# Optimization experiments

Hardware: AMD Instinct MI355X
Metric: run time of the kernel (lower is better)

## Reference

```python
import jax, jax.numpy as jnp
import numpy as np

EPS = 1e-07
B, N = 128, 512


def setup_inputs() -> dict:
    key = jax.random.key(0)
    k1, k2, k3 = jax.random.split(key, 3)
    pred = jax.random.normal(k1, (B, N), dtype=jnp.float32)
    target = jax.random.uniform(k2, (B, N), dtype=jnp.float32)  # survival times in (0,1)
    valid_mask = jax.random.bernoulli(k3, p=0.9, shape=(B, N))  # bool
    return {"pred": pred, "target": target, "valid_mask": valid_mask}


def reference(pred, target, valid_mask):
    # pred, target: (B, N) float32; valid_mask: (B, N) bool
    n = pred.shape[1]
    target_masked = jnp.where(valid_mask, target, jnp.float32(-1.0))  # (B, N)
    T_i = target_masked[:, :, None]  # (B, N, 1)
    T_j = target_masked[:, None, :]  # (B, 1, N)
    batch_max_time = jnp.max(target_masked, axis=1, keepdims=True)[:, :, None]  # (B, 1, 1)

    # player i is eliminated (not the final survivor) and valid
    is_elimination = (T_i < batch_max_time) & (T_i > 0) & valid_mask[:, :, None]  # (B, N, 1)
    # risk set at time t_i: players j still alive (T_j >= T_i) and valid
    risk_set_mask = (T_j >= T_i) & valid_mask[:, None, :]  # (B, N, N)

    pred_j = pred[:, None, :]  # (B, 1, N)
    risk_pred_masked = jnp.where(risk_set_mask, pred_j, -jnp.inf)  # (B, N, N)
    log_denominator = jax.nn.logsumexp(risk_pred_masked, axis=2, keepdims=True)  # (B, N, 1)
    log_probs = pred_j - log_denominator  # (B, N, N)

    # part 1: -log p of the eliminated player itself (diagonal)
    log_prob_eliminated = jnp.diagonal(log_probs, axis1=1, axis2=2)[:, :, None]  # (B, N, 1)
    loss_part1 = -log_prob_eliminated * is_elimination

    # part 2: -log(1 - p_i) for survivors i in risk set (excluding eliminated)
    probs = jnp.exp(log_probs)
    eye = jnp.eye(n, dtype=bool)[None]  # (1, N, N)
    surviving_mask = risk_set_mask & ~eye
    probs_clamped = jnp.minimum(probs, 1.0 - EPS)
    loss_surviving = -jnp.log(1.0 - probs_clamped + EPS)
    loss_part2 = jnp.sum(loss_surviving * surviving_mask.astype(pred.dtype), axis=2, keepdims=True)
    loss_part2 = loss_part2 * is_elimination

    total_loss_per_batch = jnp.sum(loss_part1 + loss_part2, axis=1)  # (B, 1)
    valid_batch_mask = (jnp.sum(valid_mask, axis=1) >= 2).astype(pred.dtype)  # (B,)
    final_loss = jnp.sum(jnp.squeeze(total_loss_per_batch, axis=1) * valid_batch_mask)
    num_valid = jnp.maximum(jnp.sum(valid_batch_mask), 1.0)
    return final_loss / num_valid
```

## Files before the change

kernel.cpp:

```cpp
#include <hip/hip_runtime.h>
#include <math.h>

#define BB 128
#define NN 512
#define CHUNKS 8
#define RPB (NN / CHUNKS)
#define RPW (RPB / 4)
#define GRID (BB * CHUNKS)
#define EPSF 1e-7f
#define ONEP (1.0f + EPSF)
#define TWOEPS (2.0f * EPSF)

__global__ __launch_bounds__(256) void cox_main(const float* __restrict__ pred,
                                                const float* __restrict__ target,
                                                const int* __restrict__ valid,
                                                float* __restrict__ ws) {
    __shared__ float s_e[NN];
    __shared__ float s_tm[NN];
    __shared__ float s_p[NN];
    __shared__ float s_is[NN];
    __shared__ float s_max[4];
    __shared__ float s_cnt[4];
    __shared__ float s_acc[4];

    const int b     = blockIdx.x / CHUNKS;
    const int chunk = blockIdx.x % CHUNKS;
    const int tid   = threadIdx.x;
    const int lane  = tid & 63;
    const int wave  = tid >> 6;

    float lmax = -1.0f, lcnt = 0.0f;
    #pragma unroll
    for (int k = 0; k < NN / 256; ++k) {
        int j = tid + 256 * k;
        float p = pred[b * NN + j];
        float t = target[b * NN + j];
        int   v = valid[b * NN + j];
        float tm = v ? t : -1.0f;
        s_p[j]  = p;
        s_e[j]  = __expf(p);
        s_tm[j] = tm;
        lmax = fmaxf(lmax, tm);
        lcnt += v ? 1.0f : 0.0f;
    }
    #pragma unroll
    for (int off = 32; off; off >>= 1) {
        lmax = fmaxf(lmax, __shfl_xor(lmax, off, 64));
        lcnt += __shfl_xor(lcnt, off, 64);
    }
    if (lane == 0) { s_max[wave] = lmax; s_cnt[wave] = lcnt; }
    __syncthreads();
    const float bmax = fmaxf(fmaxf(s_max[0], s_max[1]), fmaxf(s_max[2], s_max[3]));
    const float bcnt = s_cnt[0] + s_cnt[1] + s_cnt[2] + s_cnt[3];
    const float batch_valid = (bcnt >= 2.0f) ? 1.0f : 0.0f;

    float tj[8], e0[8];
    #pragma unroll
    for (int k = 0; k < 8; ++k) {
        tj[k] = s_tm[lane + 64 * k];
        e0[k] = s_e[lane + 64 * k];
    }

    float acc = 0.0f;
    const int row0 = chunk * RPB + wave * RPW;
    for (int r = 0; r < RPW; ++r) {
        const int i = row0 + r;
        const float Ti = s_tm[i];
        if (!(Ti > 0.0f && Ti < bmax)) continue;

        float em[8];
        float S = 0.0f;
        #pragma unroll
        for (int k = 0; k < 8; ++k) {
            float x = (tj[k] >= Ti) ? e0[k] : 0.0f;
            em[k] = x;
            S += x;
        }
        #pragma unroll
        for (int off = 32; off; off >>= 1) S += __shfl_xor(S, off, 64);
        const float invS = __builtin_amdgcn_rcpf(S);
        if (lane == 0) s_is[i] = invS;

        float prod = 1.0f;
        #pragma unroll
        for (int k = 0; k < 8; ++k)
            prod *= fmaxf(fmaf(-em[k], invS, ONEP), TWOEPS);
        acc -= __logf(prod);
    }

    if (lane < RPW) {
        const int i = row0 + lane;
        const float Ti = s_tm[i];
        if (Ti > 0.0f && Ti < bmax) {
            float invS = s_is[i];
            float part1 = -__logf(invS) - s_p[i];
            float pii = s_e[i] * invS;
            float qi = fmaxf(ONEP - pii, TWOEPS);
            acc += part1 + __logf(qi);
        }
    }

    #pragma unroll
    for (int off = 32; off; off >>= 1) acc += __shfl_xor(acc, off, 64);
    if (lane == 0) s_acc[wave] = acc;
    __syncthreads();
    if (tid == 0) {
        ws[blockIdx.x] = (s_acc[0] + s_acc[1] + s_acc[2] + s_acc[3]) * batch_valid;
        if (chunk == 0) ws[GRID + b] = batch_valid;
    }
}

__global__ __launch_bounds__(256) void cox_final(const float* __restrict__ ws,
                                                 float* __restrict__ out) {
    __shared__ float s_tot[4];
    __shared__ float s_cnt[4];
    const int tid  = threadIdx.x;
    const int lane = tid & 63;
    const int wave = tid >> 6;

    float tot = 0.0f;
    #pragma unroll
    for (int k = 0; k < GRID / 256; ++k) tot += ws[tid + 256 * k];
    float cnt = (tid < BB) ? ws[GRID + tid] : 0.0f;

    #pragma unroll
    for (int off = 32; off; off >>= 1) {
        tot += __shfl_xor(tot, off, 64);
        cnt += __shfl_xor(cnt, off, 64);
    }
    if (lane == 0) { s_tot[wave] = tot; s_cnt[wave] = cnt; }
    __syncthreads();
    if (tid == 0) {
        float T = s_tot[0] + s_tot[1] + s_tot[2] + s_tot[3];
        float C = s_cnt[0] + s_cnt[1] + s_cnt[2] + s_cnt[3];
        out[0] = T / fmaxf(C, 1.0f);
    }
}

extern "C" void kernel_launch(void* const* d_in, const int* in_sizes, int n_in,
                              void* d_out, int out_size, void* d_ws, size_t ws_size,
                              hipStream_t stream) {
    const float* pred   = (const float*)d_in[0];
    const float* target = (const float*)d_in[1];
    const int*   valid  = (const int*)d_in[2];
    float* out = (float*)d_out;
    float* ws  = (float*)d_ws;

    cox_main<<<GRID, 256, 0, stream>>>(pred, target, valid, ws);
    cox_final<<<1, 256, 0, stream>>>(ws, out);
}
```

Baseline: 69.29 us.

## Fold diagonal term into per-row product and process two rows branch-free

Computes the diagonal -log p_i and the +log q_i correction inside the main row loop. It does this by multiplying a factor F = invS*e_i/q_ii into the lane that owns column i, so only one log per lane per row is needed. This removes the s_p/s_is shared arrays and the separate epilogue pass. Rows are processed two at a time without the early-continue, using masking (Ti=inf, elim weight) to give more ILP across the shuffle reductions. In exchange it computes full work for non-eliminated rows, adds an extra rcp per row, and combines the terms in a different floating-point order.

New measurement: 68.95 us. About the same (-0.5%).

```diff
diff --git a/kernel.cpp b/kernel.cpp
--- a/kernel.cpp
+++ b/kernel.cpp
@@ -17,8 +17,6 @@
                                                 float* __restrict__ ws) {
     __shared__ float s_e[NN];
     __shared__ float s_tm[NN];
-    __shared__ float s_p[NN];
-    __shared__ float s_is[NN];
     __shared__ float s_max[4];
     __shared__ float s_cnt[4];
     __shared__ float s_acc[4];
@@ -37,7 +35,6 @@
         float t = target[b * NN + j];
         int   v = valid[b * NN + j];
         float tm = v ? t : -1.0f;
-        s_p[j]  = p;
         s_e[j]  = __expf(p);
         s_tm[j] = tm;
         lmax = fmaxf(lmax, tm);
@@ -63,40 +60,56 @@
 
     float acc = 0.0f;
     const int row0 = chunk * RPB + wave * RPW;
-    for (int r = 0; r < RPW; ++r) {
-        const int i = row0 + r;
-        const float Ti = s_tm[i];
-        if (!(Ti > 0.0f && Ti < bmax)) continue;
-
-        float em[8];
-        float S = 0.0f;
+    for (int r0 = 0; r0 < RPW; r0 += 2) {
+        float Ti[2], ei[2], elim[2], S[2], prod[2];
+        float em[2][8];
+        #pragma unroll
+        for (int rr = 0; rr < 2; ++rr) {
+            const int i = row0 + r0 + rr;
+            float t = s_tm[i];
+            bool el = (t > 0.0f && t < bmax);
+            elim[rr] = el ? 1.0f : 0.0f;
+            Ti[rr]   = el ? t : INFINITY;
+            ei[rr]   = s_e[i];
+            S[rr]    = 0.0f;
+            prod[rr] = 1.0f;
+        }
         #pragma unroll
         for (int k = 0; k < 8; ++k) {
-            float x = (tj[k] >= Ti) ? e0[k] : 0.0f;
-            em[k] = x;
-            S += x;
+            #pragma unroll
+            for (int rr = 0; rr < 2; ++rr) {
+                float x = (tj[k] >= Ti[rr]) ? e0[k] : 0.0f;
+                em[rr][k] = x;
+                S[rr] += x;
+            }
         }
         #pragma unroll
-        for (int off = 32; off; off >>= 1) S += __shfl_xor(S, off, 64);
-        const float invS = __builtin_amdgcn_rcpf(S);
-        if (lane == 0) s_is[i] = invS;
-
-        float prod = 1.0f;
+        for (int off = 32; off; off >>= 1) {
+            #pragma unroll
+            for (int rr = 0; rr < 2; ++rr)
+                S[rr] += __shfl_xor(S[rr], off, 64);
+        }
+        float invS[2], F[2];
         #pragma unroll
-        for (int k = 0; k < 8; ++k)
-            prod *= fmaxf(fmaf(-em[k], invS, ONEP), TWOEPS);
-        acc -= __logf(prod);
-    }
-
-    if (lane < RPW) {
-        const int i = row0 + lane;
-        const float Ti = s_tm[i];
-        if (Ti > 0.0f && Ti < bmax) {
-            float invS = s_is[i];
-            float part1 = -__logf(invS) - s_p[i];
-            float pii = s_e[i] * invS;
-            float qi = fmaxf(ONEP - pii, TWOEPS);
-            acc += part1 + __logf(qi);
+        for (int rr = 0; rr < 2; ++rr) {
+            float Sc = (elim[rr] != 0.0f) ? S[rr] : 1.0f;
+            float is = __builtin_amdgcn_rcpf(Sc);
+            invS[rr] = is;
+            float qii = fmaxf(fmaf(-ei[rr], is, ONEP), TWOEPS);
+            F[rr] = is * ei[rr] * __builtin_amdgcn_rcpf(qii);
+        }
+        #pragma unroll
+        for (int k = 0; k < 8; ++k) {
+            #pragma unroll
+            for (int rr = 0; rr < 2; ++rr)
+                prod[rr] *= fmaxf(fmaf(-em[rr][k], invS[rr], ONEP), TWOEPS);
+        }
+        #pragma unroll
+        for (int rr = 0; rr < 2; ++rr) {
+            const int i = row0 + r0 + rr;
+            float mul = (lane == (i & 63)) ? F[rr] : 1.0f;
+            prod[rr] *= mul;
+            acc -= elim[rr] * __logf(prod[rr]);
         }
     }
 
```
